# Kernel optimization log

Hardware: AMD Instinct MI355X
Metric: run time of the kernel (lower is better)

The kernel has to match this reference:

```python
import jax, jax.numpy as jnp
import numpy as np

B, DIN, H, DOUT = 8192, 1024, 2048, 1024
P, E = 4, 6            # n_patches, n_edges
C = H // P             # per-patch feature dim = 512
IDX_I = jnp.array([0, 0, 0, 1, 1, 2])  # i<j pair order matches nested loop
IDX_J = jnp.array([1, 2, 3, 2, 3, 3])


def setup_inputs() -> dict:
    key = jax.random.key(0)
    ks = jax.random.split(key, 12)
    s = 0.02
    return {
        "x": jax.random.normal(ks[0], (B, DIN), jnp.float32),
        "fiber": jax.random.normal(ks[1], (B, C), jnp.float32),  # randn_like(base) in torch fwd
        "W_in": jax.random.normal(ks[2], (DIN, H), jnp.float32) * s,
        "b_in": jnp.zeros((H,), jnp.float32),
        "incidence": jax.random.normal(ks[3], (E, P), jnp.float32) * 0.1,
        "sheaf_maps": jnp.tile((jnp.eye(C, dtype=jnp.float32) * 0.1)[None], (E, 1, 1)),
        "damping": jnp.float32(0.1),
        "Wb": jax.random.normal(ks[4], (P, C, C // 2), jnp.float32) * s,
        "bb": jnp.zeros((P, C // 2), jnp.float32),
        "Wf": jax.random.normal(ks[5], (P, C, C // 2), jnp.float32) * s,
        "bf": jnp.zeros((P, C // 2), jnp.float32),
        "Wt": jax.random.normal(ks[6], (C, C), jnp.float32) * s,
        "bt": jnp.zeros((C,), jnp.float32),
        "Wr": jax.random.normal(ks[7], (E, C, C // 2), jnp.float32) * s,
        "br": jnp.zeros((E, C // 2), jnp.float32),
        "Wg": jax.random.normal(ks[8], (H, H), jnp.float32) * s,
        "bg": jnp.zeros((H,), jnp.float32),
        "Wc": jax.random.normal(ks[9], (H + C, DOUT), jnp.float32) * s,
        "bc": jnp.zeros((DOUT,), jnp.float32),
    }


def reference(x, fiber, W_in, b_in, incidence, sheaf_maps, damping,
              Wb, bb, Wf, bf, Wt, bt, Wr, br, Wg, bg, Wc, bc):
    # input projection + split into P contiguous chunks (stack == reshape)
    h = x @ W_in + b_in                                      # [B, H]
    sections = h.reshape(B, P, C)                            # [B, P, C]

    # --- NeuralSheafLaplacian ---
    # coboundary: incidence-weighted combination of patch sections, then per-edge sheaf map
    weighted = jnp.einsum('ep,bpc->bec', incidence, sections)          # [B, E, C]
    coboundary = jnp.einsum('bec,ecd->bed', weighted, sheaf_maps)      # [B, E, C]
    L = incidence.T @ incidence                                        # [P, P] = delta^T delta
    diffused = sections - damping * jnp.einsum('pq,bqc->bpc', L, sections)
    h1_norm = jnp.linalg.norm(coboundary, axis=-1).mean(axis=-1)       # [B]

    # --- FiberBundleLayer ---
    base = diffused.mean(axis=1)                                       # [B, C]
    b_proj = jnp.einsum('bc,scd->bsd', base, Wb) + bb                  # [B, P, C/2]
    f_proj = jnp.einsum('bc,scd->bsd', fiber, Wf) + bf                 # [B, P, C/2]
    simplices = jnp.concatenate([b_proj, f_proj], axis=-1) @ Wt + bt   # [B, P, C]
    total = simplices.mean(axis=1)                                     # [B, C]

    # --- CohomologyConsistency ---
    si = diffused[:, IDX_I]                                            # [B, E, C]
    sj = diffused[:, IDX_J]                                            # [B, E, C]
    ri = jnp.einsum('bec,ecd->bed', si, Wr) + br
    rj = jnp.einsum('bec,ecd->bed', sj, Wr) + br
    h1_loss = jnp.mean((ri - rj) ** 2, axis=(0, 2)).mean()             # mean of per-pair MSEs
    glued = diffused.reshape(B, H) @ Wg + bg                           # cat(sections) == reshape

    output = jnp.concatenate([glued, total], axis=-1) @ Wc + bc        # [B, DOUT]
    return output, diffused, h1_norm, h1_loss, total
```

## Files before the change

kernel.cpp:

```cpp
#include <hip/hip_runtime.h>
#include <cstdint>

#define B_    8192
#define DIN_  1024
#define H_    2048
#define DOUT_ 1024
#define P4_   4
#define E6_   6
#define C_    512
#define C2_   256

typedef __bf16 bf16x8 __attribute__((ext_vector_type(8)));
typedef float  f32x4  __attribute__((ext_vector_type(4)));

__device__ __forceinline__ unsigned short f2bf_bits(float f) {
    unsigned u = __float_as_uint(f);
    unsigned r = (u + 0x7fffu + ((u >> 16) & 1u)) >> 16;
    return (unsigned short)r;
}
__device__ __forceinline__ float bf2f(unsigned short s) {
    return __uint_as_float(((unsigned)s) << 16);
}

__device__ __forceinline__ void async_load16(void* lds, const void* g) {
    __builtin_amdgcn_global_load_lds(
        (__attribute__((address_space(1))) void*)(uintptr_t)g,
        (__attribute__((address_space(3))) void*)(unsigned int)(uintptr_t)lds,
        16, 0, 0);
}


__global__ void convert_f32_bf16_k(const float* __restrict__ in,
                                   unsigned short* __restrict__ out, int n) {
    int i = (blockIdx.x * blockDim.x + threadIdx.x) * 4;
    if (i + 3 < n) {
        float4 v = *(const float4*)(in + i);
        ushort4 o;
        o.x = f2bf_bits(v.x); o.y = f2bf_bits(v.y);
        o.z = f2bf_bits(v.z); o.w = f2bf_bits(v.w);
        *(ushort4*)(out + i) = o;
    }
}

__global__ void transpose_to_bf16_k(const float* __restrict__ in,
                                    unsigned short* __restrict__ out,
                                    int R, int Cc, long inStrideZ, long outStrideZ) {
    __shared__ float t[32][33];
    in  += (long)blockIdx.z * inStrideZ;
    out += (long)blockIdx.z * outStrideZ;
    int x0 = blockIdx.x << 5, y0 = blockIdx.y << 5;
    int tx = threadIdx.x, ty = threadIdx.y;
#pragma unroll
    for (int j = 0; j < 32; j += 8)
        t[ty + j][tx] = in[(long)(y0 + ty + j) * Cc + x0 + tx];
    __syncthreads();
#pragma unroll
    for (int j = 0; j < 32; j += 8)
        out[(long)(x0 + ty + j) * R + y0 + tx] = f2bf_bits(t[tx][ty + j]);
}

__global__ void wbar_k(const float* __restrict__ W, unsigned short* __restrict__ outT) {
    int id = blockIdx.x * blockDim.x + threadIdx.x;
    int d = id >> 9, c = id & 511;
    float s = 0.f;
#pragma unroll
    for (int si = 0; si < 4; si++) s += W[si * (512 * 256) + c * 256 + d];
    outT[id] = f2bf_bits(0.25f * s);
}

__global__ void bbar_k(const float* __restrict__ b, float* __restrict__ out) {
    int d = threadIdx.x;
    out[d] = 0.25f * (b[d] + b[256 + d] + b[512 + d] + b[768 + d]);
}

__global__ void k2_diffuse_k(const unsigned short* __restrict__ hb,
                             const float* __restrict__ incidence,
                             const float* __restrict__ damping,
                             float* __restrict__ outDiff,
                             unsigned short* __restrict__ diffb,
                             unsigned short* __restrict__ baseb,
                             unsigned short* __restrict__ weightedb,
                             unsigned short* __restrict__ debuf) {
    __shared__ float M4[4][4];
    __shared__ float inc2[24];
    int tid = threadIdx.x;
    if (tid < 16) {
        int p = tid >> 2, q = tid & 3;
        float l = 0.f;
#pragma unroll
        for (int e = 0; e < 6; e++) l += incidence[e * 4 + p] * incidence[e * 4 + q];
        M4[p][q] = (p == q ? 1.f : 0.f) - damping[0] * l;
    }
    if (tid < 24) inc2[tid] = incidence[tid];
    __syncthreads();

    int b = blockIdx.x >> 1;
    int c = ((blockIdx.x & 1) << 8) + tid;
    long hoff = (long)b * H_ + c;
    float s0 = bf2f(hb[hoff]);
    float s1 = bf2f(hb[hoff + 512]);
    float s2 = bf2f(hb[hoff + 1024]);
    float s3 = bf2f(hb[hoff + 1536]);

    float d0 = M4[0][0]*s0 + M4[0][1]*s1 + M4[0][2]*s2 + M4[0][3]*s3;
    float d1 = M4[1][0]*s0 + M4[1][1]*s1 + M4[1][2]*s2 + M4[1][3]*s3;
    float d2 = M4[2][0]*s0 + M4[2][1]*s1 + M4[2][2]*s2 + M4[2][3]*s3;
    float d3 = M4[3][0]*s0 + M4[3][1]*s1 + M4[3][2]*s2 + M4[3][3]*s3;

    outDiff[hoff]        = d0;
    outDiff[hoff + 512]  = d1;
    outDiff[hoff + 1024] = d2;
    outDiff[hoff + 1536] = d3;
    diffb[hoff]        = f2bf_bits(d0);
    diffb[hoff + 512]  = f2bf_bits(d1);
    diffb[hoff + 1024] = f2bf_bits(d2);
    diffb[hoff + 1536] = f2bf_bits(d3);
    baseb[(long)b * C_ + c] = f2bf_bits(0.25f * (d0 + d1 + d2 + d3));

#pragma unroll
    for (int e = 0; e < 6; e++) {
        float w = inc2[e*4+0]*s0 + inc2[e*4+1]*s1 + inc2[e*4+2]*s2 + inc2[e*4+3]*s3;
        weightedb[(long)e * (B_ * (long)C_) + (long)b * C_ + c] = f2bf_bits(w);
    }
    float dI[6] = {d0, d0, d0, d1, d1, d2};
    float dJ[6] = {d1, d2, d3, d2, d3, d3};
#pragma unroll
    for (int e = 0; e < 6; e++)
        debuf[(long)e * (B_ * (long)C_) + (long)b * C_ + c] = f2bf_bits(dI[e] - dJ[e]);
}

template <int MODE>
__global__ __launch_bounds__(256, 2)
void gemm_bt_k(const unsigned short* __restrict__ A, long sAz, int lda,
               const unsigned short* __restrict__ Bt, long sBz, int K,
               const float* __restrict__ bias,
               unsigned short* __restrict__ Cb, int ldcb,
               float* __restrict__ Cf, int ldcf,
               float* __restrict__ red, long sRz) {
    __shared__ __align__(16) unsigned short smA[128 * 64];
    __shared__ __align__(16) unsigned short smB[128 * 64];
    const int tid = threadIdx.x;
    const int lane = tid & 63, w = tid >> 6;
    const int wm = w >> 1, wn = w & 1;
    const int m16 = lane & 15, quad = lane >> 4;
    const int m7 = m16 & 7;
    A  += (long)blockIdx.z * sAz;
    Bt += (long)blockIdx.z * sBz;
    const long rowA0 = (long)blockIdx.y * 128;
    const long rowB0 = (long)blockIdx.x * 128;

    f32x4 acc[4][4];
#pragma unroll
    for (int i = 0; i < 4; i++)
#pragma unroll
        for (int j = 0; j < 4; j++) acc[i][j] = f32x4{0.f, 0.f, 0.f, 0.f};

    for (int k0 = 0; k0 < K; k0 += 64) {
#pragma unroll
        for (int i = 0; i < 4; i++) {
            int chunk = i * 256 + tid;
            int row = chunk >> 3;
            int keS = ((chunk & 7) ^ (row & 7)) << 3;
            async_load16(&smA[chunk << 3], A  + (rowA0 + row) * (long)lda + k0 + keS);
            async_load16(&smB[chunk << 3], Bt + (rowB0 + row) * (long)K   + k0 + keS);
        }
        __syncthreads();
#pragma unroll
        for (int kk = 0; kk < 64; kk += 32) {
            const int pc = (((kk >> 3) + quad) ^ m7) << 3;
            bf16x8 af[4], bfv[4];
#pragma unroll
            for (int i = 0; i < 4; i++) {
                af[i]  = *(const bf16x8*)&smA[((wm << 6) + (i << 4) + m16) * 64 + pc];
                bfv[i] = *(const bf16x8*)&smB[((wn << 6) + (i << 4) + m16) * 64 + pc];
            }
#pragma unroll
            for (int i = 0; i < 4; i++)
#pragma unroll
                for (int j = 0; j < 4; j++)
                    acc[i][j] = __builtin_amdgcn_mfma_f32_16x16x32_bf16(af[i], bfv[j], acc[i][j], 0, 0, 0);
        }
        __syncthreads();
    }

    const long rowBase = rowA0 + (wm << 6);
    const long colBase = rowB0 + (wn << 6);

    if (MODE <= 2) {
#pragma unroll
        for (int j = 0; j < 4; j++) {
            long col = colBase + (j << 4) + m16;
            float bv = bias ? bias[col] : 0.f;
#pragma unroll
            for (int i = 0; i < 4; i++) {
                long row = rowBase + (i << 4) + (quad << 2);
#pragma unroll
                for (int r = 0; r < 4; r++) {
                    float v = acc[i][j][r] + bv;
                    if (MODE == 0 || MODE == 2) Cb[(row + r) * (long)ldcb + col] = f2bf_bits(v);
                    if (MODE == 1 || MODE == 2) Cf[(row + r) * (long)ldcf + col] = v;
                }
            }
        }
    } else if (MODE == 3) {
        float* rz = red + (long)blockIdx.z * sRz;
#pragma unroll
        for (int i = 0; i < 4; i++) {
            float v0 = 0.f, v1 = 0.f, v2 = 0.f, v3 = 0.f;
#pragma unroll
            for (int j = 0; j < 4; j++) {
                float a0 = acc[i][j][0], a1 = acc[i][j][1], a2 = acc[i][j][2], a3 = acc[i][j][3];
                v0 += a0 * a0; v1 += a1 * a1; v2 += a2 * a2; v3 += a3 * a3;
            }
#pragma unroll
            for (int m = 1; m <= 8; m <<= 1) {
                v0 += __shfl_xor(v0, m); v1 += __shfl_xor(v1, m);
                v2 += __shfl_xor(v2, m); v3 += __shfl_xor(v3, m);
            }
            if (m16 == 0) {
                long row = rowBase + (i << 4) + (quad << 2);
                atomicAdd(&rz[row + 0], v0);
                atomicAdd(&rz[row + 1], v1);
                atomicAdd(&rz[row + 2], v2);
                atomicAdd(&rz[row + 3], v3);
            }
        }
    } else {
        float s = 0.f;
#pragma unroll
        for (int i = 0; i < 4; i++)
#pragma unroll
            for (int j = 0; j < 4; j++)
#pragma unroll
                for (int r = 0; r < 4; r++) { float a = acc[i][j][r]; s += a * a; }
#pragma unroll
        for (int m = 1; m <= 32; m <<= 1) s += __shfl_xor(s, m);
        if (lane == 0) atomicAdd(red, s);
    }
}

__global__ void f1_h1norm_k(const float* __restrict__ hn, float* __restrict__ out) {
    int b = blockIdx.x * 256 + threadIdx.x;
    float s = 0.f;
#pragma unroll
    for (int e = 0; e < 6; e++) s += sqrtf(hn[e * B_ + b]);
    out[b] = s * (1.f / 6.f);
}

__global__ void f2_h1loss_k(const float* __restrict__ acc, float* __restrict__ out) {
    if (threadIdx.x == 0) out[0] = acc[0] * (1.f / (8192.f * 6.f * 256.f));
}

extern "C" void kernel_launch(void* const* d_in, const int* in_sizes, int n_in,
                              void* d_out, int out_size, void* d_ws, size_t ws_size,
                              hipStream_t stream) {
    const float* x     = (const float*)d_in[0];
    const float* fiber = (const float*)d_in[1];
    const float* W_in  = (const float*)d_in[2];
    const float* b_in  = (const float*)d_in[3];
    const float* incid = (const float*)d_in[4];
    const float* sheaf = (const float*)d_in[5];
    const float* damp  = (const float*)d_in[6];
    const float* Wb    = (const float*)d_in[7];
    const float* bb    = (const float*)d_in[8];
    const float* Wf    = (const float*)d_in[9];
    const float* bfv   = (const float*)d_in[10];
    const float* Wt    = (const float*)d_in[11];
    const float* bt    = (const float*)d_in[12];
    const float* Wr    = (const float*)d_in[13];
    const float* Wg    = (const float*)d_in[15];
    const float* bg    = (const float*)d_in[16];
    const float* Wc    = (const float*)d_in[17];
    const float* bc    = (const float*)d_in[18];

    float* out      = (float*)d_out;
    float* outDiff  = out + 8388608;
    float* outH1n   = out + 25165824;
    float* outH1l   = out + 25174016;
    float* outTotal = out + 25174017;

    char* ws = (char*)d_ws;
    size_t o = 0;
    auto alloc = [&](size_t bytes) { size_t r = o; o += (bytes + 255) & ~(size_t)255; return r; };

    size_t r0 = alloc(50331648);
    unsigned short* xb = (unsigned short*)(ws + r0);
    unsigned short* hb = (unsigned short*)(ws + r0 + 16777216);
    unsigned short* Ab = (unsigned short*)(ws + r0);
    unsigned short* diffb     = (unsigned short*)(ws + alloc(33554432));
    unsigned short* baseb     = (unsigned short*)(ws + alloc(8388608));
    unsigned short* weightedb = (unsigned short*)(ws + alloc(50331648));
    unsigned short* debuf     = (unsigned short*)(ws + alloc(50331648));
    unsigned short* fiberb    = (unsigned short*)(ws + alloc(8388608));
    unsigned short* cbar      = (unsigned short*)(ws + alloc(8388608));
    unsigned short* WinT   = (unsigned short*)(ws + alloc(4194304));
    unsigned short* WgT    = (unsigned short*)(ws + alloc(8388608));
    unsigned short* WcT    = (unsigned short*)(ws + alloc(5242880));
    unsigned short* WtT    = (unsigned short*)(ws + alloc(524288));
    unsigned short* WrT    = (unsigned short*)(ws + alloc(1572864));
    unsigned short* ShT    = (unsigned short*)(ws + alloc(3145728));
    unsigned short* WbBarT = (unsigned short*)(ws + alloc(262144));
    unsigned short* WfBarT = (unsigned short*)(ws + alloc(262144));
    float* bbarf  = (float*)(ws + alloc(1024));
    float* bfbarf = (float*)(ws + alloc(1024));
    float* hnacc  = (float*)(ws + alloc(6 * 8192 * 4 + 256));
    float* lossacc = hnacc + 6 * 8192;

    (void)hipMemsetAsync(hnacc, 0, 6 * 8192 * 4 + 256, stream);

    convert_f32_bf16_k<<<8192, 256, 0, stream>>>(x, xb, 8388608);
    convert_f32_bf16_k<<<4096, 256, 0, stream>>>(fiber, fiberb, 4194304);
    dim3 tb(32, 8);
    transpose_to_bf16_k<<<dim3(64, 32), tb, 0, stream>>>(W_in, WinT, 1024, 2048, 0, 0);
    transpose_to_bf16_k<<<dim3(64, 64), tb, 0, stream>>>(Wg, WgT, 2048, 2048, 0, 0);
    transpose_to_bf16_k<<<dim3(32, 80), tb, 0, stream>>>(Wc, WcT, 2560, 1024, 0, 0);
    transpose_to_bf16_k<<<dim3(16, 16), tb, 0, stream>>>(Wt, WtT, 512, 512, 0, 0);
    transpose_to_bf16_k<<<dim3(16, 16, 6), tb, 0, stream>>>(sheaf, ShT, 512, 512, 512 * 512, 512 * 512);
    transpose_to_bf16_k<<<dim3(8, 16, 6), tb, 0, stream>>>(Wr, WrT, 512, 256, 512 * 256, 512 * 256);
    wbar_k<<<512, 256, 0, stream>>>(Wb, WbBarT);
    wbar_k<<<512, 256, 0, stream>>>(Wf, WfBarT);
    bbar_k<<<1, 256, 0, stream>>>(bb, bbarf);
    bbar_k<<<1, 256, 0, stream>>>(bfv, bfbarf);

    gemm_bt_k<0><<<dim3(16, 64, 1), 256, 0, stream>>>(xb, 0, DIN_, WinT, 0, DIN_,
                                                      b_in, hb, H_, nullptr, 0, nullptr, 0);
    k2_diffuse_k<<<16384, 256, 0, stream>>>(hb, incid, damp, outDiff, diffb, baseb, weightedb, debuf);

    gemm_bt_k<0><<<dim3(16, 64, 1), 256, 0, stream>>>(diffb, 0, H_, WgT, 0, H_,
                                                      bg, Ab, 2560, nullptr, 0, nullptr, 0);
    gemm_bt_k<3><<<dim3(4, 64, 6), 256, 0, stream>>>(weightedb, (long)B_ * C_, C_, ShT, (long)C_ * C_, C_,
                                                     nullptr, nullptr, 0, nullptr, 0, hnacc, B_);
    gemm_bt_k<4><<<dim3(2, 64, 6), 256, 0, stream>>>(debuf, (long)B_ * C_, C_, WrT, (long)C2_ * C_, C_,
                                                     nullptr, nullptr, 0, nullptr, 0, lossacc, 0);
    gemm_bt_k<0><<<dim3(2, 64, 1), 256, 0, stream>>>(baseb, 0, C_, WbBarT, 0, C_,
                                                     bbarf, cbar, C_, nullptr, 0, nullptr, 0);
    gemm_bt_k<0><<<dim3(2, 64, 1), 256, 0, stream>>>(fiberb, 0, C_, WfBarT, 0, C_,
                                                     bfbarf, cbar + 256, C_, nullptr, 0, nullptr, 0);
    gemm_bt_k<2><<<dim3(4, 64, 1), 256, 0, stream>>>(cbar, 0, C_, WtT, 0, C_,
                                                     bt, Ab + 2048, 2560, outTotal, C_, nullptr, 0);
    gemm_bt_k<1><<<dim3(8, 64, 1), 256, 0, stream>>>(Ab, 0, 2560, WcT, 0, 2560,
                                                     bc, nullptr, 0, out, DOUT_, nullptr, 0);
    f1_h1norm_k<<<32, 256, 0, stream>>>(hnacc, outH1n);
    f2_h1loss_k<<<1, 64, 0, stream>>>(lossacc, outH1l);

    (void)in_sizes; (void)n_in; (void)out_size; (void)ws_size;
}
```

Baseline: 608.8 us.

## Fold diffusion matrix and Wg into Wc to eliminate the glue GEMM

```diff
diff --git a/kernel.cpp b/kernel.cpp
--- a/kernel.cpp
+++ b/kernel.cpp
@@ -68,16 +68,67 @@
     outT[id] = f2bf_bits(0.25f * s);
 }
 
-__global__ void bbar_k(const float* __restrict__ b, float* __restrict__ out) {
-    int d = threadIdx.x;
-    out[d] = 0.25f * (b[d] + b[256 + d] + b[512 + d] + b[768 + d]);
-}
-
-__global__ void k2_diffuse_k(const unsigned short* __restrict__ hb,
+__global__ void bbar2_k(const float* __restrict__ bb, const float* __restrict__ bfv,
+                        float* __restrict__ o1, float* __restrict__ o2) {
+    int t = threadIdx.x;
+    const float* s = (t < 256) ? bb : bfv;
+    float* dst = (t < 256) ? o1 : o2;
+    int d = t & 255;
+    dst[d] = 0.25f * (s[d] + s[256 + d] + s[512 + d] + s[768 + d]);
+}
+
+__global__ void fold_wg_k(const float* __restrict__ Wg,
+                          const float* __restrict__ incidence,
+                          const float* __restrict__ damping,
+                          unsigned short* __restrict__ Wgp) {
+    __shared__ float M4[16];
+    int tid = threadIdx.x;
+    if (tid < 16) {
+        int p = tid >> 2, q = tid & 3;
+        float l = 0.f;
+#pragma unroll
+        for (int e = 0; e < 6; e++) l += incidence[e * 4 + p] * incidence[e * 4 + q];
+        M4[tid] = (p == q ? 1.f : 0.f) - damping[0] * l;
+    }
+    __syncthreads();
+    long idx = (long)blockIdx.x * 256 + tid;
+    int k = (int)(idx >> 9);
+    int j = (int)(idx & 511) << 2;
+    int q = k >> 9, c = k & 511;
+    float4 r0 = *(const float4*)(Wg + ((long)(0 * 512 + c)) * 2048 + j);
+    float4 r1 = *(const float4*)(Wg + ((long)(1 * 512 + c)) * 2048 + j);
+    float4 r2 = *(const float4*)(Wg + ((long)(2 * 512 + c)) * 2048 + j);
+    float4 r3 = *(const float4*)(Wg + ((long)(3 * 512 + c)) * 2048 + j);
+    float m0 = M4[0 * 4 + q], m1 = M4[1 * 4 + q], m2 = M4[2 * 4 + q], m3 = M4[3 * 4 + q];
+    ushort4 o;
+    o.x = f2bf_bits(m0 * r0.x + m1 * r1.x + m2 * r2.x + m3 * r3.x);
+    o.y = f2bf_bits(m0 * r0.y + m1 * r1.y + m2 * r2.y + m3 * r3.y);
+    o.z = f2bf_bits(m0 * r0.z + m1 * r1.z + m2 * r2.z + m3 * r3.z);
+    o.w = f2bf_bits(m0 * r0.w + m1 * r1.w + m2 * r2.w + m3 * r3.w);
+    *(ushort4*)(Wgp + (long)k * 2048 + j) = o;
+}
+
+__global__ void copy_wcbot_k(const unsigned short* __restrict__ WcT,
+                             unsigned short* __restrict__ BtG7) {
+    int idx = blockIdx.x * 256 + threadIdx.x;
+    int n = idx >> 6;
+    int k = (idx & 63) << 3;
+    long off = (long)n * 2560 + 2048 + k;
+    *(uint4*)(BtG7 + off) = *(const uint4*)(WcT + off);
+}
+
+__global__ void bias_out_k(const float* __restrict__ Wc, const float* __restrict__ bg,
+                           const float* __restrict__ bc, float* __restrict__ bout) {
+    int n = blockIdx.x * 256 + threadIdx.x;
+    float s = bc[n];
+    for (int j = 0; j < 2048; j++) s += bg[j] * Wc[(long)j * 1024 + n];
+    bout[n] = s;
+}
+
+__global__ void k2_diffuse_k(const unsigned short* __restrict__ Ab,
                              const float* __restrict__ incidence,
                              const float* __restrict__ damping,
                              float* __restrict__ outDiff,
-                             unsigned short* __restrict__ diffb,
                              unsigned short* __restrict__ baseb,
                              unsigned short* __restrict__ weightedb,
                              unsigned short* __restrict__ debuf) {
@@ -96,25 +147,22 @@
 
     int b = blockIdx.x >> 1;
     int c = ((blockIdx.x & 1) << 8) + tid;
-    long hoff = (long)b * H_ + c;
-    float s0 = bf2f(hb[hoff]);
-    float s1 = bf2f(hb[hoff + 512]);
-    float s2 = bf2f(hb[hoff + 1024]);
-    float s3 = bf2f(hb[hoff + 1536]);
+    long aoff = (long)b * 2560 + c;
+    long doff = (long)b * H_ + c;
+    float s0 = bf2f(Ab[aoff]);
+    float s1 = bf2f(Ab[aoff + 512]);
+    float s2 = bf2f(Ab[aoff + 1024]);
+    float s3 = bf2f(Ab[aoff + 1536]);
 
     float d0 = M4[0][0]*s0 + M4[0][1]*s1 + M4[0][2]*s2 + M4[0][3]*s3;
     float d1 = M4[1][0]*s0 + M4[1][1]*s1 + M4[1][2]*s2 + M4[1][3]*s3;
     float d2 = M4[2][0]*s0 + M4[2][1]*s1 + M4[2][2]*s2 + M4[2][3]*s3;
     float d3 = M4[3][0]*s0 + M4[3][1]*s1 + M4[3][2]*s2 + M4[3][3]*s3;
 
-    outDiff[hoff]        = d0;
-    outDiff[hoff + 512]  = d1;
-    outDiff[hoff + 1024] = d2;
-    outDiff[hoff + 1536] = d3;
-    diffb[hoff]        = f2bf_bits(d0);
-    diffb[hoff + 512]  = f2bf_bits(d1);
-    diffb[hoff + 1024] = f2bf_bits(d2);
-    diffb[hoff + 1536] = f2bf_bits(d3);
+    outDiff[doff]        = d0;
+    outDiff[doff + 512]  = d1;
+    outDiff[doff + 1024] = d2;
+    outDiff[doff + 1536] = d3;
     baseb[(long)b * C_ + c] = f2bf_bits(0.25f * (d0 + d1 + d2 + d3));
 
 #pragma unroll
@@ -133,9 +181,9 @@
 __global__ __launch_bounds__(256, 2)
 void gemm_bt_k(const unsigned short* __restrict__ A, long sAz, int lda,
                const unsigned short* __restrict__ Bt, long sBz, int K,
-               const float* __restrict__ bias,
-               unsigned short* __restrict__ Cb, int ldcb,
-               float* __restrict__ Cf, int ldcf,
+               const float* __restrict__ bias, long sBiasZ,
+               unsigned short* __restrict__ Cb, int ldcb, long sCbz,
+               float* __restrict__ Cf, int ldcf, long sCfz,
                float* __restrict__ red, long sRz) {
     __shared__ __align__(16) unsigned short smA[128 * 64];
     __shared__ __align__(16) unsigned short smB[128 * 64];
@@ -146,6 +194,9 @@
     const int m7 = m16 & 7;
     A  += (long)blockIdx.z * sAz;
     Bt += (long)blockIdx.z * sBz;
+    if (bias) bias += (long)blockIdx.z * sBiasZ;
+    if (Cb)   Cb   += (long)blockIdx.z * sCbz;
+    if (Cf)   Cf   += (long)blockIdx.z * sCfz;
     const long rowA0 = (long)blockIdx.y * 128;
     const long rowB0 = (long)blockIdx.x * 128;
 
@@ -283,26 +334,25 @@
     size_t o = 0;
     auto alloc = [&](size_t bytes) { size_t r = o; o += (bytes + 255) & ~(size_t)255; return r; };
 
-    size_t r0 = alloc(50331648);
-    unsigned short* xb = (unsigned short*)(ws + r0);
-    unsigned short* hb = (unsigned short*)(ws + r0 + 16777216);
-    unsigned short* Ab = (unsigned short*)(ws + r0);
-    unsigned short* diffb     = (unsigned short*)(ws + alloc(33554432));
+    unsigned short* Ab        = (unsigned short*)(ws + alloc(41943040));
+    unsigned short* xb        = (unsigned short*)(ws + alloc(16777216));
     unsigned short* baseb     = (unsigned short*)(ws + alloc(8388608));
+    unsigned short* fiberb    = (unsigned short*)(ws + alloc(8388608));
     unsigned short* weightedb = (unsigned short*)(ws + alloc(50331648));
     unsigned short* debuf     = (unsigned short*)(ws + alloc(50331648));
-    unsigned short* fiberb    = (unsigned short*)(ws + alloc(8388608));
     unsigned short* cbar      = (unsigned short*)(ws + alloc(8388608));
     unsigned short* WinT   = (unsigned short*)(ws + alloc(4194304));
-    unsigned short* WgT    = (unsigned short*)(ws + alloc(8388608));
     unsigned short* WcT    = (unsigned short*)(ws + alloc(5242880));
     unsigned short* WtT    = (unsigned short*)(ws + alloc(524288));
     unsigned short* WrT    = (unsigned short*)(ws + alloc(1572864));
     unsigned short* ShT    = (unsigned short*)(ws + alloc(3145728));
     unsigned short* WbBarT = (unsigned short*)(ws + alloc(262144));
     unsigned short* WfBarT = (unsigned short*)(ws + alloc(262144));
+    unsigned short* Wgp    = (unsigned short*)(ws + alloc(8388608));
+    unsigned short* BtG7   = (unsigned short*)(ws + alloc(5242880));
     float* bbarf  = (float*)(ws + alloc(1024));
     float* bfbarf = (float*)(ws + alloc(1024));
+    float* bout   = (float*)(ws + alloc(4096));
     float* hnacc  = (float*)(ws + alloc(6 * 8192 * 4 + 256));
     float* lossacc = hnacc + 6 * 8192;
 
@@ -312,34 +362,41 @@
     convert_f32_bf16_k<<<4096, 256, 0, stream>>>(fiber, fiberb, 4194304);
     dim3 tb(32, 8);
     transpose_to_bf16_k<<<dim3(64, 32), tb, 0, stream>>>(W_in, WinT, 1024, 2048, 0, 0);
-    transpose_to_bf16_k<<<dim3(64, 64), tb, 0, stream>>>(Wg, WgT, 2048, 2048, 0, 0);
     transpose_to_bf16_k<<<dim3(32, 80), tb, 0, stream>>>(Wc, WcT, 2560, 1024, 0, 0);
     transpose_to_bf16_k<<<dim3(16, 16), tb, 0, stream>>>(Wt, WtT, 512, 512, 0, 0);
     transpose_to_bf16_k<<<dim3(16, 16, 6), tb, 0, stream>>>(sheaf, ShT, 512, 512, 512 * 512, 512 * 512);
     transpose_to_bf16_k<<<dim3(8, 16, 6), tb, 0, stream>>>(Wr, WrT, 512, 256, 512 * 256, 512 * 256);
     wbar_k<<<512, 256, 0, stream>>>(Wb, WbBarT);
     wbar_k<<<512, 256, 0, stream>>>(Wf, WfBarT);
-    bbar_k<<<1, 256, 0, stream>>>(bb, bbarf);
-    bbar_k<<<1, 256, 0, stream>>>(bfv, bfbarf);
+    bbar2_k<<<1, 512, 0, stream>>>(bb, bfv, bbarf, bfbarf);
+    fold_wg_k<<<4096, 256, 0, stream>>>(Wg, incid, damp, Wgp);
+    bias_out_k<<<4, 256, 0, stream>>>(Wc, bg, bc, bout);
+
+    gemm_bt_k<0><<<dim3(16, 8, 1), 256, 0, stream>>>(WcT, 0, 2560, Wgp, 0, 2048,
+                                                     nullptr, 0, BtG7, 2560, 0,
+                                                     nullptr, 0, 0, nullptr, 0);
+    copy_wcbot_k<<<256, 256, 0, stream>>>(WcT, BtG7);
 
     gemm_bt_k<0><<<dim3(16, 64, 1), 256, 0, stream>>>(xb, 0, DIN_, WinT, 0, DIN_,
-                                                      b_in, hb, H_, nullptr, 0, nullptr, 0);
-    k2_diffuse_k<<<16384, 256, 0, stream>>>(hb, incid, damp, outDiff, diffb, baseb, weightedb, debuf);
-
-    gemm_bt_k<0><<<dim3(16, 64, 1), 256, 0, stream>>>(diffb, 0, H_, WgT, 0, H_,
-                                                      bg, Ab, 2560, nullptr, 0, nullptr, 0);
+                                                      b_in, 0, Ab, 2560, 0,
+                                                      nullptr, 0, 0, nullptr, 0);
+    k2_diffuse_k<<<16384, 256, 0, stream>>>(Ab, incid, damp, outDiff, baseb, weightedb, debuf);
+
     gemm_bt_k<3><<<dim3(4, 64, 6), 256, 0, stream>>>(weightedb, (long)B_ * C_, C_, ShT, (long)C_ * C_, C_,
-                                                     nullptr, nullptr, 0, nullptr, 0, hnacc, B_);
+                                                     nullptr, 0, nullptr, 0, 0,
+                                                     nullptr, 0, 0, hnacc, B_);
     gemm_bt_k<4><<<dim3(2, 64, 6), 256, 0, stream>>>(debuf, (long)B_ * C_, C_, WrT, (long)C2_ * C_, C_,
-                                                     nullptr, nullptr, 0, nullptr, 0, lossacc, 0);
-    gemm_bt_k<0><<<dim3(2, 64, 1), 256, 0, stream>>>(baseb, 0, C_, WbBarT, 0, C_,
-                                                     bbarf, cbar, C_, nullptr, 0, nullptr, 0);
-    gemm_bt_k<0><<<dim3(2, 64, 1), 256, 0, stream>>>(fiberb, 0, C_, WfBarT, 0, C_,
-                                                     bfbarf, cbar + 256, C_, nullptr, 0, nullptr, 0);
+                                                     nullptr, 0, nullptr, 0, 0,
+                                                     nullptr, 0, 0, lossacc, 0);
+    gemm_bt_k<0><<<dim3(2, 64, 2), 256, 0, stream>>>(baseb, 4194304, C_, WbBarT, 131072, C_,
+                                                     bbarf, 256, cbar, C_, 256,
+                                                     nullptr, 0, 0, nullptr, 0);
     gemm_bt_k<2><<<dim3(4, 64, 1), 256, 0, stream>>>(cbar, 0, C_, WtT, 0, C_,
-                                                     bt, Ab + 2048, 2560, outTotal, C_, nullptr, 0);
-    gemm_bt_k<1><<<dim3(8, 64, 1), 256, 0, stream>>>(Ab, 0, 2560, WcT, 0, 2560,
-                                                     bc, nullptr, 0, out, DOUT_, nullptr, 0);
+                                                     bt, 0, Ab + 2048, 2560, 0,
+                                                     outTotal, C_, 0, nullptr, 0);
+    gemm_bt_k<1><<<dim3(8, 64, 1), 256, 0, stream>>>(Ab, 0, 2560, BtG7, 0, 2560,
+                                                     bout, 0, nullptr, 0, 0,
+                                                     out, DOUT_, 0, nullptr, 0);
     f1_h1norm_k<<<32, 256, 0, stream>>>(hnacc, outH1n);
     f2_h1loss_k<<<1, 64, 0, stream>>>(lossacc, outH1l);
 
```

Result: slower. 637.2 us (+4.7%).
